# Optimization experiments

Hardware: AMD Instinct MI355X
Metric: run time of the kernel (lower is better)

Reference implementation:

```python
import jax, jax.numpy as jnp
import numpy as np

N, D, E = 50000, 128, 800000
NEG_SLOPE = 0.2


def setup_inputs() -> dict:
    key = jax.random.key(0)
    ks = jax.random.split(key, 16)
    src = jax.random.randint(ks[0], (E,), 0, N)
    dst = jax.random.randint(ks[1], (E,), 0, N)
    dst = jnp.where(src == dst, (dst + 1) % N, dst)  # no pre-existing self loops (PyG strips them)
    edge_index = jnp.stack([src, dst]).astype(jnp.int32)
    s = 1.0 / np.sqrt(D)  # glorot-ish scale
    return {
        'edge_index': edge_index,
        'embed': jax.random.normal(ks[2], (N, D), jnp.float32),
        'Wl1': jax.random.normal(ks[3], (D, D), jnp.float32) * s,
        'bl1': jnp.zeros((D,), jnp.float32),
        'Wr1': jax.random.normal(ks[4], (D, D), jnp.float32) * s,
        'br1': jnp.zeros((D,), jnp.float32),
        'att1': jax.random.normal(ks[5], (4, D // 4), jnp.float32) * s,
        'b1': jnp.zeros((D,), jnp.float32),
        'Wl2': jax.random.normal(ks[6], (D, D), jnp.float32) * s,
        'bl2': jnp.zeros((D,), jnp.float32),
        'Wr2': jax.random.normal(ks[7], (D, D), jnp.float32) * s,
        'br2': jnp.zeros((D,), jnp.float32),
        'att2': jax.random.normal(ks[8], (1, D), jnp.float32) * s,
        'b2': jnp.zeros((D,), jnp.float32),
    }


def gatv2(x, src, dst, Wl, bl, Wr, br, att, bias, heads, out_ch):
    n = x.shape[0]
    xl = (x @ Wl + bl).reshape(n, heads, out_ch)  # source-side messages
    xr = (x @ Wr + br).reshape(n, heads, out_ch)  # target-side
    e = jax.nn.leaky_relu(xl[src] + xr[dst], NEG_SLOPE)      # [E, H, C]
    score = jnp.einsum('ehc,hc->eh', e, att)                  # [E, H]
    # segment softmax over incoming edges of each target node
    smax = jax.ops.segment_max(score, dst, num_segments=n)
    ex = jnp.exp(score - smax[dst])
    denom = jax.ops.segment_sum(ex, dst, num_segments=n)
    alpha = ex / (denom[dst] + 1e-16)                         # [E, H]
    out = jax.ops.segment_sum(xl[src] * alpha[:, :, None], dst, num_segments=n)
    return out.reshape(n, heads * out_ch) + bias


def reference(edge_index, embed, Wl1, bl1, Wr1, br1, att1, b1,
              Wl2, bl2, Wr2, br2, att2, b2):
    loops = jnp.arange(N, dtype=edge_index.dtype)
    src = jnp.concatenate([edge_index[0], loops])  # add_self_loops=True (PyG default)
    dst = jnp.concatenate([edge_index[1], loops])
    x = gatv2(embed, src, dst, Wl1, bl1, Wr1, br1, att1, b1, 4, D // 4)
    x = jax.nn.relu(x)
    return gatv2(x, src, dst, Wl2, bl2, Wr2, br2, att2, b2, 1, D)
```

## Files before the change

kernel.cpp:

```cpp
#include <hip/hip_runtime.h>
#include <hip/hip_bf16.h>

#define NEG_SLOPE 0.2f
#define CAP 80

typedef unsigned short u16;
typedef short v8s __attribute__((ext_vector_type(8)));
typedef float v4f __attribute__((ext_vector_type(4)));

__device__ __forceinline__ u16 f32_to_bf16(float f) {
    unsigned u = __float_as_uint(f);
    u += 0x7fffu + ((u >> 16) & 1u);
    return (u16)(u >> 16);
}
__device__ __forceinline__ float4 bf16x4_to_f4(uint2 u) {
    float4 f;
    f.x = __uint_as_float(u.x << 16);
    f.y = __uint_as_float(u.x & 0xffff0000u);
    f.z = __uint_as_float(u.y << 16);
    f.w = __uint_as_float(u.y & 0xffff0000u);
    return f;
}

__global__ __launch_bounds__(256)
void prep(const float* __restrict__ Wa, const float* __restrict__ Wb,
          const float* __restrict__ Wc, const float* __restrict__ Wd,
          u16* __restrict__ dst, int* __restrict__ cnt, int n)
{
    int g = blockIdx.x * 256 + threadIdx.x;
    if (g < n) cnt[g] = 0;
    if (g >= 8192) return;
    int mat = g >> 11, rem = g & 2047;
    int f = rem >> 6, lane = rem & 63;
    int kt = f >> 3, nt = f & 7, q = lane >> 4, c = lane & 15;
    const float* W = (mat == 0) ? Wa : (mat == 1) ? Wb : (mat == 2) ? Wc : Wd;
    unsigned pk[4];
    #pragma unroll
    for (int jj = 0; jj < 4; ++jj) {
        float a = W[(kt * 32 + q * 8 + 2 * jj    ) * 128 + nt * 16 + c];
        float b = W[(kt * 32 + q * 8 + 2 * jj + 1) * 128 + nt * 16 + c];
        pk[jj] = (unsigned)f32_to_bf16(a) | ((unsigned)f32_to_bf16(b) << 16);
    }
    uint4 o; o.x = pk[0]; o.y = pk[1]; o.z = pk[2]; o.w = pk[3];
    *reinterpret_cast<uint4*>(dst + (size_t)mat * 16384 + ((size_t)f * 64 + lane) * 8) = o;
}

__global__ __launch_bounds__(256)
void scatter_slots(const int* __restrict__ esrc, const int* __restrict__ edst,
                   int e_in, int e_tot, int* __restrict__ cnt,
                   int* __restrict__ slots)
{
    int e = blockIdx.x * 256 + threadIdx.x;
    if (e >= e_tot) return;
    int s, d;
    if (e < e_in) { s = esrc[e]; d = edst[e]; } else { s = e - e_in; d = s; }
    int pos = atomicAdd(&cnt[d], 1);
    if (pos < CAP) slots[(size_t)d * CAP + pos] = s;
}

template<bool BF16_IN>
__global__ __launch_bounds__(256)
void gemm_mfma(const void* __restrict__ xin,
               const v8s* __restrict__ pwl, const v8s* __restrict__ pwr,
               const float* __restrict__ bl, const float* __restrict__ br,
               u16* __restrict__ outl, u16* __restrict__ outr, int n)
{
    __shared__ u16 xs[64 * 136];
    const int tid = threadIdx.x;
    const int node0 = blockIdx.x * 64;

    #pragma unroll
    for (int it = 0; it < 8; ++it) {
        int flat4 = it * 256 + tid;
        int row = flat4 >> 5;
        int col = (flat4 & 31) * 4;
        uint2 w = make_uint2(0u, 0u);
        if (node0 + row < n) {
            if (BF16_IN) {
                w = *reinterpret_cast<const uint2*>(
                        (const u16*)xin + (size_t)(node0 + row) * 128 + col);
            } else {
                float4 v = *reinterpret_cast<const float4*>(
                        (const float*)xin + (size_t)(node0 + row) * 128 + col);
                w.x = (unsigned)f32_to_bf16(v.x) | ((unsigned)f32_to_bf16(v.y) << 16);
                w.y = (unsigned)f32_to_bf16(v.z) | ((unsigned)f32_to_bf16(v.w) << 16);
            }
        }
        *reinterpret_cast<uint2*>(&xs[row * 136 + col]) = w;
    }
    __syncthreads();

    const int lane = tid & 63;
    const int wv   = tid >> 6;
    const int mat  = wv & 1;
    const int ch   = wv >> 1;
    const int q = lane >> 4, c = lane & 15;

    const v8s* __restrict__ pw     = mat ? pwr : pwl;
    const float* __restrict__ bias = mat ? br : bl;
    u16* __restrict__ outp         = mat ? outr : outl;

    v8s bfr[4][4];
    #pragma unroll
    for (int kt = 0; kt < 4; ++kt)
        #pragma unroll
        for (int nt = 0; nt < 4; ++nt)
            bfr[kt][nt] = pw[(kt * 8 + ch * 4 + nt) * 64 + lane];

    float bcol[4];
    #pragma unroll
    for (int nt = 0; nt < 4; ++nt) bcol[nt] = bias[ch * 64 + nt * 16 + c];

    #pragma unroll
    for (int mt = 0; mt < 4; ++mt) {
        const int arow = mt * 16 + c;
        v8s a[4];
        #pragma unroll
        for (int kt = 0; kt < 4; ++kt)
            a[kt] = *reinterpret_cast<const v8s*>(&xs[arow * 136 + kt * 32 + q * 8]);

        v4f acc0 = {0.f, 0.f, 0.f, 0.f};
        v4f acc1 = {0.f, 0.f, 0.f, 0.f};
        v4f acc2 = {0.f, 0.f, 0.f, 0.f};
        v4f acc3 = {0.f, 0.f, 0.f, 0.f};
        #pragma unroll
        for (int kt = 0; kt < 4; ++kt) {
            acc0 = __builtin_amdgcn_mfma_f32_16x16x32_bf16(a[kt], bfr[kt][0], acc0, 0, 0, 0);
            acc1 = __builtin_amdgcn_mfma_f32_16x16x32_bf16(a[kt], bfr[kt][1], acc1, 0, 0, 0);
            acc2 = __builtin_amdgcn_mfma_f32_16x16x32_bf16(a[kt], bfr[kt][2], acc2, 0, 0, 0);
            acc3 = __builtin_amdgcn_mfma_f32_16x16x32_bf16(a[kt], bfr[kt][3], acc3, 0, 0, 0);
        }

        #pragma unroll
        for (int r = 0; r < 4; ++r) {
            int node = node0 + mt * 16 + q * 4 + r;
            if (node < n) {
                size_t rb = (size_t)node * 128;
                outp[rb + ch * 64 +  0 + c] = f32_to_bf16(acc0[r] + bcol[0]);
                outp[rb + ch * 64 + 16 + c] = f32_to_bf16(acc1[r] + bcol[1]);
                outp[rb + ch * 64 + 32 + c] = f32_to_bf16(acc2[r] + bcol[2]);
                outp[rb + ch * 64 + 48 + c] = f32_to_bf16(acc3[r] + bcol[3]);
            }
        }
    }
}

template<int H>
__device__ __forceinline__ float edge_ex(float4 xlv, float4 xrv, float4 atv)
{
    float4 t = make_float4(xlv.x + xrv.x, xlv.y + xrv.y,
                           xlv.z + xrv.z, xlv.w + xrv.w);
    t.x = t.x > 0.f ? t.x : NEG_SLOPE * t.x;
    t.y = t.y > 0.f ? t.y : NEG_SLOPE * t.y;
    t.z = t.z > 0.f ? t.z : NEG_SLOPE * t.z;
    t.w = t.w > 0.f ? t.w : NEG_SLOPE * t.w;
    float p = t.x * atv.x + t.y * atv.y + t.z * atv.z + t.w * atv.w;
    p += __shfl_xor(p, 1);
    p += __shfl_xor(p, 2);
    p += __shfl_xor(p, 4);
    if (H == 1) {
        p += __shfl_xor(p, 8);
        p += __shfl_xor(p, 16);
    }
    return __expf(p);
}

template<int H, bool RELU_BF16_OUT>
__global__ __launch_bounds__(256)
void fused_attn(const u16* __restrict__ xl, const u16* __restrict__ xr,
                const float* __restrict__ att, const int* __restrict__ slots,
                const int* __restrict__ cnt, const float* __restrict__ bias,
                void* __restrict__ outv, int n)
{
    int d = blockIdx.x * 8 + (threadIdx.x >> 5);
    if (d >= n) return;
    const int lane = threadIdx.x & 31;

    const float4 xrv = bf16x4_to_f4(
        *reinterpret_cast<const uint2*>(&xr[(size_t)d * 128 + lane * 4]));
    const float4 atv = *reinterpret_cast<const float4*>(&att[lane * 4]);

    const int start = d * CAP;
    const int end   = start + min(cnt[d], CAP);

    float4 acc0 = make_float4(0.f, 0.f, 0.f, 0.f);
    float4 acc1 = make_float4(0.f, 0.f, 0.f, 0.f);
    float4 acc2 = make_float4(0.f, 0.f, 0.f, 0.f);
    float4 acc3 = make_float4(0.f, 0.f, 0.f, 0.f);
    float  den0 = 0.f, den1 = 0.f, den2 = 0.f, den3 = 0.f;

    for (int base = start; base < end; base += 32) {
        const int cnt32 = min(32, end - base);
        int sidx = (base + lane < end) ? slots[base + lane] : 0;
        int i = 0;
        for (; i + 4 <= cnt32; i += 4) {
            int s0 = __shfl(sidx, i, 32);
            int s1 = __shfl(sidx, i + 1, 32);
            int s2 = __shfl(sidx, i + 2, 32);
            int s3 = __shfl(sidx, i + 3, 32);
            float4 x0 = bf16x4_to_f4(*reinterpret_cast<const uint2*>(&xl[(size_t)s0 * 128 + lane * 4]));
            float4 x1 = bf16x4_to_f4(*reinterpret_cast<const uint2*>(&xl[(size_t)s1 * 128 + lane * 4]));
            float4 x2 = bf16x4_to_f4(*reinterpret_cast<const uint2*>(&xl[(size_t)s2 * 128 + lane * 4]));
            float4 x3 = bf16x4_to_f4(*reinterpret_cast<const uint2*>(&xl[(size_t)s3 * 128 + lane * 4]));
            float ex0 = edge_ex<H>(x0, xrv, atv);
            float ex1 = edge_ex<H>(x1, xrv, atv);
            float ex2 = edge_ex<H>(x2, xrv, atv);
            float ex3 = edge_ex<H>(x3, xrv, atv);
            den0 += ex0;
            acc0.x = fmaf(x0.x, ex0, acc0.x);
            acc0.y = fmaf(x0.y, ex0, acc0.y);
            acc0.z = fmaf(x0.z, ex0, acc0.z);
            acc0.w = fmaf(x0.w, ex0, acc0.w);
            den1 += ex1;
            acc1.x = fmaf(x1.x, ex1, acc1.x);
            acc1.y = fmaf(x1.y, ex1, acc1.y);
            acc1.z = fmaf(x1.z, ex1, acc1.z);
            acc1.w = fmaf(x1.w, ex1, acc1.w);
            den2 += ex2;
            acc2.x = fmaf(x2.x, ex2, acc2.x);
            acc2.y = fmaf(x2.y, ex2, acc2.y);
            acc2.z = fmaf(x2.z, ex2, acc2.z);
            acc2.w = fmaf(x2.w, ex2, acc2.w);
            den3 += ex3;
            acc3.x = fmaf(x3.x, ex3, acc3.x);
            acc3.y = fmaf(x3.y, ex3, acc3.y);
            acc3.z = fmaf(x3.z, ex3, acc3.z);
            acc3.w = fmaf(x3.w, ex3, acc3.w);
        }
        for (; i < cnt32; ++i) {
            int s0 = __shfl(sidx, i, 32);
            float4 x0 = bf16x4_to_f4(*reinterpret_cast<const uint2*>(&xl[(size_t)s0 * 128 + lane * 4]));
            float ex0 = edge_ex<H>(x0, xrv, atv);
            den0 += ex0;
            acc0.x = fmaf(x0.x, ex0, acc0.x);
            acc0.y = fmaf(x0.y, ex0, acc0.y);
            acc0.z = fmaf(x0.z, ex0, acc0.z);
            acc0.w = fmaf(x0.w, ex0, acc0.w);
        }
    }

    const float inv = 1.f / (den0 + den1 + den2 + den3 + 1e-16f);
    const float4 bv = *reinterpret_cast<const float4*>(&bias[lane * 4]);
    float4 r = make_float4((acc0.x + acc1.x + acc2.x + acc3.x) * inv + bv.x,
                           (acc0.y + acc1.y + acc2.y + acc3.y) * inv + bv.y,
                           (acc0.z + acc1.z + acc2.z + acc3.z) * inv + bv.z,
                           (acc0.w + acc1.w + acc2.w + acc3.w) * inv + bv.w);
    if (RELU_BF16_OUT) {
        r.x = fmaxf(r.x, 0.f); r.y = fmaxf(r.y, 0.f);
        r.z = fmaxf(r.z, 0.f); r.w = fmaxf(r.w, 0.f);
        uint2 o;
        o.x = (unsigned)f32_to_bf16(r.x) | ((unsigned)f32_to_bf16(r.y) << 16);
        o.y = (unsigned)f32_to_bf16(r.z) | ((unsigned)f32_to_bf16(r.w) << 16);
        *reinterpret_cast<uint2*>((u16*)outv + (size_t)d * 128 + lane * 4) = o;
    } else {
        *reinterpret_cast<float4*>((float*)outv + (size_t)d * 128 + lane * 4) = r;
    }
}


extern "C" void kernel_launch(void* const* d_in, const int* in_sizes, int n_in,
                              void* d_out, int out_size, void* d_ws, size_t ws_size,
                              hipStream_t stream)
{
    const int*   edge  = (const int*)d_in[0];
    const float* embed = (const float*)d_in[1];
    const float* Wl1   = (const float*)d_in[2];
    const float* bl1   = (const float*)d_in[3];
    const float* Wr1   = (const float*)d_in[4];
    const float* br1   = (const float*)d_in[5];
    const float* att1  = (const float*)d_in[6];
    const float* b1    = (const float*)d_in[7];
    const float* Wl2   = (const float*)d_in[8];
    const float* bl2   = (const float*)d_in[9];
    const float* Wr2   = (const float*)d_in[10];
    const float* br2   = (const float*)d_in[11];
    const float* att2  = (const float*)d_in[12];
    const float* b2    = (const float*)d_in[13];

    const int e_in  = in_sizes[0] / 2;
    const int n     = in_sizes[1] / 128;
    const int e_tot = e_in + n;

    char* p = (char*)d_ws;
    u16* xl    = (u16*)p;  p += (size_t)n * 128 * 2;
    u16* xr    = (u16*)p;  p += (size_t)n * 128 * 2;
    u16* h1    = (u16*)p;  p += (size_t)n * 128 * 2;
    u16* wpack = (u16*)p;  p += (size_t)4 * 16384 * 2;
    int* cnt   = (int*)p;  p += (size_t)n * 4;
    int* slots = (int*)p;
    float* out = (float*)d_out;

    const int* esrc = edge;
    const int* edst = edge + e_in;

    dim3 blk(256);
    const int gemm_blocks = (n + 63) / 64;
    const int node_blocks = (n + 7) / 8;
    const int edge_blocks = (e_tot + 255) / 256;
    const int prep_blocks = (n + 255) / 256;

    prep<<<prep_blocks, blk, 0, stream>>>(Wl1, Wr1, Wl2, Wr2, wpack, cnt, n);
    scatter_slots<<<edge_blocks, blk, 0, stream>>>(esrc, edst, e_in, e_tot, cnt, slots);

    gemm_mfma<false><<<gemm_blocks, blk, 0, stream>>>(
        embed, (const v8s*)wpack, (const v8s*)(wpack + 16384),
        bl1, br1, xl, xr, n);
    fused_attn<4, true><<<node_blocks, blk, 0, stream>>>(
        xl, xr, att1, slots, cnt, b1, h1, n);

    gemm_mfma<true><<<gemm_blocks, blk, 0, stream>>>(
        h1, (const v8s*)(wpack + 32768), (const v8s*)(wpack + 49152),
        bl2, br2, xl, xr, n);
    fused_attn<1, false><<<node_blocks, blk, 0, stream>>>(
        xl, xr, att2, slots, cnt, b2, out, n);
}
```

Before: 275.1 us.

## Build per-node edge slots via two-level bucketing with LDS atomics

Replaces the direct per-destination global atomic scatter with a two-pass build. Edges are first binned into 192-node buckets as packed (src, local dst) words, then each bucket is expanded into slot lists using shared-memory atomics and written out with coalesced stores. The aim is to cut scattered global atomics and uncoalesced slot writes. In exchange it adds an extra kernel and a packing step. Packing src into 16 bits cannot hold node ids above 65535, and a bucket that overflows its 4096-entry cap silently drops edges.

```diff
diff --git a/kernel.cpp b/kernel.cpp
--- a/kernel.cpp
+++ b/kernel.cpp
@@ -3,6 +3,8 @@
 
 #define NEG_SLOPE 0.2f
 #define CAP 80
+#define BNODES 192
+#define BCAP 4096
 
 typedef unsigned short u16;
 typedef short v8s __attribute__((ext_vector_type(8)));
@@ -25,10 +27,10 @@
 __global__ __launch_bounds__(256)
 void prep(const float* __restrict__ Wa, const float* __restrict__ Wb,
           const float* __restrict__ Wc, const float* __restrict__ Wd,
-          u16* __restrict__ dst, int* __restrict__ cnt, int n)
+          u16* __restrict__ dst, int* __restrict__ bcur, int ncur)
 {
     int g = blockIdx.x * 256 + threadIdx.x;
-    if (g < n) cnt[g] = 0;
+    if (g < ncur) bcur[g] = 0;
     if (g >= 8192) return;
     int mat = g >> 11, rem = g & 2047;
     int f = rem >> 6, lane = rem & 63;
@@ -46,16 +48,46 @@
 }
 
 __global__ __launch_bounds__(256)
-void scatter_slots(const int* __restrict__ esrc, const int* __restrict__ edst,
-                   int e_in, int e_tot, int* __restrict__ cnt,
-                   int* __restrict__ slots)
+void bin_edges(const int* __restrict__ esrc, const int* __restrict__ edst,
+               int e_in, int e_tot, int* __restrict__ bcur,
+               unsigned* __restrict__ barr)
 {
     int e = blockIdx.x * 256 + threadIdx.x;
     if (e >= e_tot) return;
     int s, d;
     if (e < e_in) { s = esrc[e]; d = edst[e]; } else { s = e - e_in; d = s; }
-    int pos = atomicAdd(&cnt[d], 1);
-    if (pos < CAP) slots[(size_t)d * CAP + pos] = s;
+    int b  = d / BNODES;
+    int dl = d - b * BNODES;
+    int pos = atomicAdd(&bcur[b * 16], 1);
+    if (pos < BCAP)
+        barr[(size_t)b * BCAP + pos] = (unsigned)s | ((unsigned)dl << 16);
+}
+
+__global__ __launch_bounds__(256)
+void bucket_build(const unsigned* __restrict__ barr, const int* __restrict__ bcur,
+                  int* __restrict__ slots, int* __restrict__ cnt)
+{
+    __shared__ int cnt_l[BNODES];
+    __shared__ int sl[BNODES * CAP];
+    const int b = blockIdx.x;
+    const int t = threadIdx.x;
+    if (t < BNODES) cnt_l[t] = 0;
+    __syncthreads();
+
+    const int ce = min(bcur[b * 16], BCAP);
+    for (int i = t; i < ce; i += 256) {
+        unsigned u = barr[(size_t)b * BCAP + i];
+        int s  = (int)(u & 0xffffu);
+        int dl = (int)(u >> 16);
+        int pos = atomicAdd(&cnt_l[dl], 1);
+        if (pos < CAP) sl[dl * CAP + pos] = s;
+    }
+    __syncthreads();
+
+    const size_t base = (size_t)b * BNODES * CAP;
+    for (int i = t; i < BNODES * CAP; i += 256)
+        slots[base + i] = sl[i];
+    if (t < BNODES) cnt[b * BNODES + t] = min(cnt_l[t], CAP);
 }
 
 template<bool BF16_IN>
@@ -280,13 +312,16 @@
     const int e_in  = in_sizes[0] / 2;
     const int n     = in_sizes[1] / 128;
     const int e_tot = e_in + n;
+    const int NB    = (n + BNODES - 1) / BNODES;
 
     char* p = (char*)d_ws;
     u16* xl    = (u16*)p;  p += (size_t)n * 128 * 2;
     u16* xr    = (u16*)p;  p += (size_t)n * 128 * 2;
     u16* h1    = (u16*)p;  p += (size_t)n * 128 * 2;
     u16* wpack = (u16*)p;  p += (size_t)4 * 16384 * 2;
-    int* cnt   = (int*)p;  p += (size_t)n * 4;
+    int* bcur  = (int*)p;  p += (size_t)NB * 16 * 4;
+    unsigned* barr = (unsigned*)p;  p += (size_t)NB * BCAP * 4;
+    int* cnt   = (int*)p;  p += (size_t)NB * BNODES * 4;
     int* slots = (int*)p;
     float* out = (float*)d_out;
 
@@ -297,10 +332,10 @@
     const int gemm_blocks = (n + 63) / 64;
     const int node_blocks = (n + 7) / 8;
     const int edge_blocks = (e_tot + 255) / 256;
-    const int prep_blocks = (n + 255) / 256;
-
-    prep<<<prep_blocks, blk, 0, stream>>>(Wl1, Wr1, Wl2, Wr2, wpack, cnt, n);
-    scatter_slots<<<edge_blocks, blk, 0, stream>>>(esrc, edst, e_in, e_tot, cnt, slots);
+
+    prep<<<32, blk, 0, stream>>>(Wl1, Wr1, Wl2, Wr2, wpack, bcur, NB * 16);
+    bin_edges<<<edge_blocks, blk, 0, stream>>>(esrc, edst, e_in, e_tot, bcur, barr);
+    bucket_build<<<NB, blk, 0, stream>>>(barr, bcur, slots, cnt);
 
     gemm_mfma<false><<<gemm_blocks, blk, 0, stream>>>(
         embed, (const v8s*)wpack, (const v8s*)(wpack + 16384),
```

After: 306.6 us. +11.5%, slower.
